# Optimization experiments

Measured on AMD Instinct MI355X. Metric: run time of the kernel, lower is better.

The kernel has to match this reference:

```python
import jax, jax.numpy as jnp
import numpy as np

B, S, D = 4, 2048, 2048
NH, NKV = 16, 4
HD = D // NH            # 128
DKV = NKV * HD          # 512
REP = NH // NKV         # 4
SCALE = HD ** -0.5
EPS = 1e-9


def setup_inputs() -> dict:
    key = jax.random.key(0)
    ks = jax.random.split(key, 9)
    s = 0.02
    return {
        "q": jax.random.normal(ks[0], (B, S, D), jnp.float32),
        "k": jax.random.normal(ks[1], (B, S, D), jnp.float32),
        "v": jax.random.normal(ks[2], (B, S, D), jnp.float32),
        "Wq": jax.random.normal(ks[3], (D, D), jnp.float32) * s,
        "bq": jnp.zeros((D,), jnp.float32),
        "Wk": jax.random.normal(ks[4], (D, DKV), jnp.float32) * s,
        "bk": jnp.zeros((DKV,), jnp.float32),
        "Wv": jax.random.normal(ks[5], (D, DKV), jnp.float32) * s,
        "bv": jnp.zeros((DKV,), jnp.float32),
    }


def reference(q, k, v, Wq, bq, Wk, bk, Wv, bv):
    # Dense projections (nn.Dense = x @ W + b)
    qh = q @ Wq + bq                      # (B, S, D)
    kh = k @ Wk + bk                      # (B, S, DKV)
    vh = v @ Wv + bv                      # (B, S, DKV)
    # Faithful to source: repeat along axis=-2 (the SEQUENCE axis)
    kh = jnp.repeat(kh, REP, axis=-2)     # (B, S*REP, DKV)
    vh = jnp.repeat(vh, REP, axis=-2)     # (B, S*REP, DKV)
    # flash_attention math: reshape to (B, S, NH, HD) -> (B, NH, S, HD)
    qh = qh.reshape(B, S, NH, HD).transpose(0, 2, 1, 3)
    kh = kh.reshape(B, S, NH, HD).transpose(0, 2, 1, 3)
    vh = vh.reshape(B, S, NH, HD).transpose(0, 2, 1, 3)
    attn = jnp.einsum("bhqd,bhkd->bhqk", qh, kh) * SCALE
    m = jnp.max(attn, axis=-1, keepdims=True)
    e = jnp.exp(attn - m)
    p = e / (jnp.sum(e, axis=-1, keepdims=True) + EPS)
    out = jnp.einsum("bhqk,bhkd->bhqd", p, vh)   # (B, NH, S, HD)
    return out.transpose(0, 2, 1, 3).reshape(B, S, D)
```

## Files before the change

kernel.cpp:

```cpp
#include <hip/hip_runtime.h>

#define B_    4
#define S_    2048
#define D_    2048
#define NH_   16
#define NKV_  4
#define HD_   128
#define DKV_  512
#define QSCALE_ ((float)(0.08838834764831845 * 1.4426950408889634))

typedef __attribute__((ext_vector_type(8))) short          bf16x8;
typedef __attribute__((ext_vector_type(8))) unsigned short us8;
typedef __attribute__((ext_vector_type(4))) unsigned short us4;
typedef __attribute__((ext_vector_type(4))) float          f32x4;

__device__ __forceinline__ unsigned short f2bf(float f) {
    union { float f; unsigned int u; } v; v.f = f;
    unsigned int u = v.u;
    u += 0x7fffu + ((u >> 16) & 1u);
    return (unsigned short)(u >> 16);
}

__device__ __forceinline__ unsigned int cvt_pk_bf16(float lo, float hi) {
    unsigned int r;
    asm volatile("v_cvt_pk_bf16_f32 %0, %1, %2" : "=v"(r) : "v"(lo), "v"(hi));
    return r;
}

#define GLOAD16(gp, lp) __builtin_amdgcn_global_load_lds(                      \
    (const __attribute__((address_space(1))) unsigned int*)(gp),              \
    (__attribute__((address_space(3))) unsigned int*)(lp), 16, 0, 0)

__device__ __forceinline__ void tr_body(
    const float* __restrict__ W, unsigned short* __restrict__ WT,
    int K, int N, int kb, int nb, float (*tile)[33])
{
    const int k0 = kb * 32, n0 = nb * 32;
    const int tx = threadIdx.x & 31, ty = threadIdx.x >> 5;
#pragma unroll
    for (int i = 0; i < 32; i += 8)
        tile[ty + i][tx] = W[(size_t)(k0 + ty + i) * N + n0 + tx];
    __syncthreads();
#pragma unroll
    for (int i = 0; i < 32; i += 8)
        WT[(size_t)(n0 + ty + i) * K + k0 + tx] = f2bf(tile[tx][ty + i]);
}

__global__ __launch_bounds__(256) void transpose_all(
    const float* __restrict__ Wq, const float* __restrict__ Wk,
    const float* __restrict__ Wv, unsigned short* __restrict__ WqT,
    unsigned short* __restrict__ WkT, unsigned short* __restrict__ WvT)
{
    __shared__ float tile[32][33];
    const int y = blockIdx.y;
    if (y < 64)       tr_body(Wq, WqT, D_, D_,   blockIdx.x, y,      tile);
    else if (y < 80)  tr_body(Wk, WkT, D_, DKV_, blockIdx.x, y - 64, tile);
    else              tr_body(Wv, WvT, D_, DKV_, blockIdx.x, y - 80, tile);
}

__device__ __forceinline__ void cvt_body(
    const float* __restrict__ src, unsigned short* __restrict__ dst, int n8)
{
    int i = blockIdx.x * blockDim.x + threadIdx.x;
    const int stride = gridDim.x * blockDim.x;
    const float4* p = (const float4*)src;
    us8* o8 = (us8*)dst;
    for (; i < n8; i += stride) {
        float4 a = p[2 * i], b = p[2 * i + 1];
        us8 o;
        o[0] = f2bf(a.x); o[1] = f2bf(a.y); o[2] = f2bf(a.z); o[3] = f2bf(a.w);
        o[4] = f2bf(b.x); o[5] = f2bf(b.y); o[6] = f2bf(b.z); o[7] = f2bf(b.w);
        o8[i] = o;
    }
}

__global__ __launch_bounds__(256) void cvt_bf16(
    const float* __restrict__ in, unsigned short* __restrict__ out, int n8)
{
    cvt_body(in, out, n8);
}

__global__ __launch_bounds__(256) void cvt_all(
    const float* __restrict__ q, const float* __restrict__ k,
    const float* __restrict__ v, unsigned short* __restrict__ xq,
    unsigned short* __restrict__ xk, unsigned short* __restrict__ xv)
{
    const int which = blockIdx.y;
    const float* src = which == 0 ? q : which == 1 ? k : v;
    unsigned short* dst = which == 0 ? xq : which == 1 ? xk : xv;
    cvt_body(src, dst, B_ * S_ * D_ / 8);
}

__device__ __forceinline__ void gemm_body(
    const unsigned short* __restrict__ A, const unsigned short* __restrict__ BT,
    const float* __restrict__ bias, unsigned short* __restrict__ C,
    int N, int nb, float scale, int vmode,
    unsigned short* As, unsigned short* Bs)
{
    const int K = D_;
    const int m0 = blockIdx.x * 128, n0 = nb * 128;
    const int t = threadIdx.x;
    const int w = t >> 6, l = t & 63, lr = l & 15, lg = l >> 4;
    const int wr = (w >> 1) * 64, wc = (w & 1) * 64;
    const int sr = t >> 2, sc = (t & 3) * 8;

    const unsigned short* aS = A + (size_t)(m0 + sr) * K + sc;
    const unsigned short* bS = BT + (size_t)(n0 + sr) * K + sc;

    f32x4 acc[4][4] = {};
    const int nk = K / 32;
    for (int kt = 0; kt < nk; ++kt) {
        __syncthreads();
        GLOAD16(aS + kt * 32,                    &As[t * 8]);
        GLOAD16(aS + (size_t)64 * K + kt * 32,   &As[2048 + t * 8]);
        GLOAD16(bS + kt * 32,                    &Bs[t * 8]);
        GLOAD16(bS + (size_t)64 * K + kt * 32,   &Bs[2048 + t * 8]);
        __syncthreads();

        bf16x8 af[4], bfv[4];
#pragma unroll
        for (int i = 0; i < 4; ++i)
            af[i] = *(const bf16x8*)&As[(wr + i * 16 + lr) * 32 + lg * 8];
#pragma unroll
        for (int i = 0; i < 4; ++i)
            bfv[i] = *(const bf16x8*)&Bs[(wc + i * 16 + lr) * 32 + lg * 8];
#pragma unroll
        for (int i = 0; i < 4; ++i)
#pragma unroll
            for (int j = 0; j < 4; ++j)
                acc[i][j] = __builtin_amdgcn_mfma_f32_16x16x32_bf16(
                    af[i], bfv[j], acc[i][j], 0, 0, 0);
    }

#pragma unroll
    for (int j = 0; j < 4; ++j) {
        const int col = n0 + wc + j * 16 + lr;
        const float bv = bias[col];
#pragma unroll
        for (int i = 0; i < 4; ++i) {
            const int row0 = m0 + wr + i * 16 + lg * 4;
            if (vmode == 0) {
#pragma unroll
                for (int r = 0; r < 4; ++r)
                    C[(size_t)(row0 + r) * N + col] = f2bf((acc[i][j][r] + bv) * scale);
            } else {
                const int bb = row0 >> 11, s0 = row0 & (S_ - 1);
                us4 hv;
#pragma unroll
                for (int r = 0; r < 4; ++r) hv[r] = f2bf((acc[i][j][r] + bv) * scale);
                *(us4*)&C[((size_t)bb * N + col) * S_ + s0] = hv;
            }
        }
    }
}

__global__ __launch_bounds__(256) void gemm_all(
    const unsigned short* __restrict__ xq, const unsigned short* __restrict__ xk,
    const unsigned short* __restrict__ xv,
    const unsigned short* __restrict__ WqT, const unsigned short* __restrict__ WkT,
    const unsigned short* __restrict__ WvT,
    const float* __restrict__ bq, const float* __restrict__ bk,
    const float* __restrict__ bv,
    unsigned short* __restrict__ qh, unsigned short* __restrict__ kh,
    unsigned short* __restrict__ vhT)
{
    __shared__ __align__(16) unsigned short As[128 * 32];
    __shared__ __align__(16) unsigned short Bs[128 * 32];
    const int y = blockIdx.y;
    if (y < 16)      gemm_body(xq, WqT, bq, qh,  D_,   y,      QSCALE_, 0, As, Bs);
    else if (y < 20) gemm_body(xk, WkT, bk, kh,  DKV_, y - 16, 1.0f,    0, As, Bs);
    else             gemm_body(xv, WvT, bv, vhT, DKV_, y - 20, 1.0f,    1, As, Bs);
}

__global__ __launch_bounds__(256) void gemm_lds(
    const unsigned short* __restrict__ A, const unsigned short* __restrict__ BT,
    const float* __restrict__ bias, unsigned short* __restrict__ C,
    int N, float scale, int vmode)
{
    __shared__ __align__(16) unsigned short As[128 * 32];
    __shared__ __align__(16) unsigned short Bs[128 * 32];
    gemm_body(A, BT, bias, C, N, blockIdx.y, scale, vmode, As, Bs);
}

template <int VMODE>
__global__ __launch_bounds__(256) void gemm_rs(
    const float* __restrict__ A, const unsigned short* __restrict__ BT,
    const float* __restrict__ bias, unsigned short* __restrict__ C,
    int M, int N, int K, float scale)
{
    __shared__ unsigned short As[128][40];
    __shared__ unsigned short Bs[128][40];

    const int m0 = blockIdx.x * 128, n0 = blockIdx.y * 128;
    const int t = threadIdx.x;
    const int sr = t >> 1, sc = (t & 1) * 16;
    const int w = t >> 6, l = t & 63, lr = l & 15, lg = l >> 4;
    const int wr = (w >> 1) * 64, wc = (w & 1) * 64;

    const float* aptr = A + (size_t)(m0 + sr) * K + sc;
    const unsigned short* bptr = BT + (size_t)(n0 + sr) * K + sc;

    float4 pa0, pa1, pa2, pa3;
    us8 pb0, pb1;
    auto prefetch = [&](int k0) {
        const float4* ap = (const float4*)(aptr + k0);
        pa0 = ap[0]; pa1 = ap[1]; pa2 = ap[2]; pa3 = ap[3];
        const us8* bp = (const us8*)(bptr + k0);
        pb0 = bp[0]; pb1 = bp[1];
    };

    f32x4 acc[4][4] = {};
    prefetch(0);
    const int nk = K / 32;
    for (int kt = 0; kt < nk; ++kt) {
        __syncthreads();
        us8 c0, c1;
        c0[0] = f2bf(pa0.x); c0[1] = f2bf(pa0.y); c0[2] = f2bf(pa0.z); c0[3] = f2bf(pa0.w);
        c0[4] = f2bf(pa1.x); c0[5] = f2bf(pa1.y); c0[6] = f2bf(pa1.z); c0[7] = f2bf(pa1.w);
        c1[0] = f2bf(pa2.x); c1[1] = f2bf(pa2.y); c1[2] = f2bf(pa2.z); c1[3] = f2bf(pa2.w);
        c1[4] = f2bf(pa3.x); c1[5] = f2bf(pa3.y); c1[6] = f2bf(pa3.z); c1[7] = f2bf(pa3.w);
        *(us8*)&As[sr][sc]     = c0;
        *(us8*)&As[sr][sc + 8] = c1;
        *(us8*)&Bs[sr][sc]     = pb0;
        *(us8*)&Bs[sr][sc + 8] = pb1;
        __syncthreads();
        if (kt + 1 < nk) prefetch((kt + 1) * 32);

        bf16x8 af[4], bfv[4];
#pragma unroll
        for (int i = 0; i < 4; ++i)
            af[i] = *(const bf16x8*)&As[wr + i * 16 + lr][lg * 8];
#pragma unroll
        for (int i = 0; i < 4; ++i)
            bfv[i] = *(const bf16x8*)&Bs[wc + i * 16 + lr][lg * 8];
#pragma unroll
        for (int i = 0; i < 4; ++i)
#pragma unroll
            for (int j = 0; j < 4; ++j)
                acc[i][j] = __builtin_amdgcn_mfma_f32_16x16x32_bf16(
                    af[i], bfv[j], acc[i][j], 0, 0, 0);
    }

#pragma unroll
    for (int j = 0; j < 4; ++j) {
        const int col = n0 + wc + j * 16 + lr;
        const float bv = bias[col];
#pragma unroll
        for (int i = 0; i < 4; ++i) {
            const int row0 = m0 + wr + i * 16 + lg * 4;
            if (VMODE == 0) {
#pragma unroll
                for (int r = 0; r < 4; ++r)
                    C[(size_t)(row0 + r) * N + col] = f2bf((acc[i][j][r] + bv) * scale);
            } else {
                const int bb = row0 >> 11, s0 = row0 & (S_ - 1);
                us4 hv;
#pragma unroll
                for (int r = 0; r < 4; ++r) hv[r] = f2bf((acc[i][j][r] + bv) * scale);
                *(us4*)&C[((size_t)bb * N + col) * S_ + s0] = hv;
            }
        }
    }
}

__global__ __launch_bounds__(256, 2) void attn_kernel(
    const unsigned short* __restrict__ qh, const unsigned short* __restrict__ kh,
    const unsigned short* __restrict__ vhT, float* __restrict__ out)
{
    __shared__ __align__(16) unsigned short Kd[2][64 * 128];
    __shared__ __align__(16) unsigned short Vd[2][128 * 64];
    __shared__ __align__(16) unsigned int   P2T[4][16 * 44];

    const int qb = blockIdx.x, h = blockIdx.y, b = blockIdx.z;
    const int g = h & (NKV_ - 1);
    const int t = threadIdx.x, w = t >> 6, l = t & 63, lr = l & 15, lg = l >> 4;
    const int q0 = qb * 128 + w * 32;

    bf16x8 qf[2][4];
#pragma unroll
    for (int rf = 0; rf < 2; ++rf) {
        const unsigned short* qrow =
            qh + ((size_t)(b * S_) + q0 + rf * 16 + lr) * D_ + h * HD_;
#pragma unroll
        for (int ko = 0; ko < 4; ++ko)
            qf[rf][ko] = *(const bf16x8*)(qrow + ko * 32 + lg * 8);
    }

    f32x4 o[2][8] = {};
    float mrow[2] = {-1e30f, -1e30f};
    float ls[2]   = {0.f, 0.f};

    const unsigned short* kb_ = kh + (size_t)b * S_ * DKV_ + g * HD_;
    const unsigned short* vb_ = vhT + ((size_t)b * DKV_ + g * HD_) * S_;

    const int kc = ((t & 15) * 8) ^ (((t >> 4) & 7) << 3);
    const int vc = ((t & 7) * 8) ^ (((t >> 3) & 7) << 3);

    auto stage = [&](int buf, int kt) {
        const unsigned short* ks = kb_ + (size_t)(kt * 64) * DKV_ + kc;
        const unsigned short* vs = vb_ + kt * 64 + vc;
#pragma unroll
        for (int i = 0; i < 4; ++i)
            GLOAD16(ks + (size_t)(i * 16 + (t >> 4)) * DKV_, &Kd[buf][i * 2048 + t * 8]);
#pragma unroll
        for (int i = 0; i < 4; ++i)
            GLOAD16(vs + (size_t)(i * 32 + (t >> 3)) * S_,   &Vd[buf][i * 2048 + t * 8]);
    };

    stage(0, 0);
    stage(1, 1);

    const int swz = (lr & 7) << 3;
    unsigned int* pw = &P2T[w][lr * 44];
    int cur = 0;
    const int NT = S_ / 64;
    for (int kt = 0; kt < NT; ++kt) {
        if (kt + 1 < NT) { asm volatile("s_waitcnt vmcnt(8)" ::: "memory"); }
        else             { asm volatile("s_waitcnt vmcnt(0)" ::: "memory"); }
        __builtin_amdgcn_s_barrier();
        __builtin_amdgcn_sched_barrier(0);

        f32x4 sa[2][4] = {};
        __builtin_amdgcn_s_setprio(1);
#pragma unroll
        for (int cf = 0; cf < 4; ++cf)
#pragma unroll
            for (int ko = 0; ko < 4; ++ko) {
                bf16x8 kf = *(const bf16x8*)
                    &Kd[cur][(cf * 16 + lr) * 128 + ((ko * 32 + lg * 8) ^ swz)];
                sa[0][cf] = __builtin_amdgcn_mfma_f32_16x16x32_bf16(kf, qf[0][ko], sa[0][cf], 0, 0, 0);
                sa[1][cf] = __builtin_amdgcn_mfma_f32_16x16x32_bf16(kf, qf[1][ko], sa[1][cf], 0, 0, 0);
            }
        __builtin_amdgcn_s_setprio(0);

        bf16x8 pa[2][2];
#pragma unroll
        for (int rf = 0; rf < 2; ++rf) {
            float mxl = fmaxf(fmaxf(fmaxf(sa[rf][0][0], sa[rf][0][1]),
                                    fmaxf(sa[rf][0][2], sa[rf][0][3])),
                              fmaxf(fmaxf(sa[rf][1][0], sa[rf][1][1]),
                                    fmaxf(sa[rf][1][2], sa[rf][1][3])));
            mxl = fmaxf(mxl, fmaxf(fmaxf(fmaxf(sa[rf][2][0], sa[rf][2][1]),
                                         fmaxf(sa[rf][2][2], sa[rf][2][3])),
                                   fmaxf(fmaxf(sa[rf][3][0], sa[rf][3][1]),
                                         fmaxf(sa[rf][3][2], sa[rf][3][3]))));
            float m = mrow[rf];
            if (!__all(mxl <= m + 8.f)) {
                float mx = fmaxf(mxl, m);
                mx = fmaxf(mx, __shfl_xor(mx, 16));
                mx = fmaxf(mx, __shfl_xor(mx, 32));
                const float al = exp2f(m - mx);
                mrow[rf] = m = mx;
                ls[rf] *= al;
#pragma unroll
                for (int r = 0; r < 4; ++r) {
                    const float a = __shfl(al, lg * 4 + r);
#pragma unroll
                    for (int df = 0; df < 8; ++df) o[rf][df][r] *= a;
                }
            }
            float p[4][4];
#pragma unroll
            for (int cf = 0; cf < 4; ++cf)
#pragma unroll
                for (int r = 0; r < 4; ++r)
                    p[cf][r] = exp2f(sa[rf][cf][r] - m);
            ls[rf] += ((p[0][0] + p[0][1]) + (p[0][2] + p[0][3]))
                    + ((p[1][0] + p[1][1]) + (p[1][2] + p[1][3]))
                    + ((p[2][0] + p[2][1]) + (p[2][2] + p[2][3]))
                    + ((p[3][0] + p[3][1]) + (p[3][2] + p[3][3]));
#pragma unroll
            for (int cf = 0; cf < 4; ++cf) {
                uint2 pk;
                pk.x = cvt_pk_bf16(p[cf][0], p[cf][1]);
                pk.y = cvt_pk_bf16(p[cf][2], p[cf][3]);
                *(uint2*)&pw[cf * 8 + lg * 2] = pk;
            }
            pa[rf][0] = *(const bf16x8*)&pw[lg * 4];
            pa[rf][1] = *(const bf16x8*)&pw[16 + lg * 4];
        }

        __builtin_amdgcn_s_setprio(1);
#pragma unroll
        for (int ks = 0; ks < 2; ++ks)
#pragma unroll
            for (int df = 0; df < 8; ++df) {
                bf16x8 vf = *(const bf16x8*)
                    &Vd[cur][(df * 16 + lr) * 64 + ((ks * 32 + lg * 8) ^ swz)];
                o[0][df] = __builtin_amdgcn_mfma_f32_16x16x32_bf16(pa[0][ks], vf, o[0][df], 0, 0, 0);
                o[1][df] = __builtin_amdgcn_mfma_f32_16x16x32_bf16(pa[1][ks], vf, o[1][df], 0, 0, 0);
            }
        __builtin_amdgcn_s_setprio(0);

        __builtin_amdgcn_sched_barrier(0);
        __builtin_amdgcn_s_barrier();
        __builtin_amdgcn_sched_barrier(0);
        if (kt + 2 < NT) stage(cur, kt + 2);
        cur ^= 1;
    }

#pragma unroll
    for (int rf = 0; rf < 2; ++rf) {
        float lst = ls[rf];
        lst += __shfl_xor(lst, 16);
        lst += __shfl_xor(lst, 32);
        const float inv = 1.f / (lst + 1e-9f);
        float* ob = out + ((size_t)(b * S_) + q0 + rf * 16 + lg * 4) * D_ + h * HD_;
#pragma unroll
        for (int r = 0; r < 4; ++r) {
            const float ivr = __shfl(inv, lg * 4 + r);
#pragma unroll
            for (int df = 0; df < 8; ++df)
                ob[(size_t)r * D_ + df * 16 + lr] = o[rf][df][r] * ivr;
        }
    }
}

extern "C" void kernel_launch(void* const* d_in, const int* in_sizes, int n_in,
                              void* d_out, int out_size, void* d_ws, size_t ws_size,
                              hipStream_t stream)
{
    const float* q  = (const float*)d_in[0];
    const float* k  = (const float*)d_in[1];
    const float* v  = (const float*)d_in[2];
    const float* Wq = (const float*)d_in[3];
    const float* bq = (const float*)d_in[4];
    const float* Wk = (const float*)d_in[5];
    const float* bk = (const float*)d_in[6];
    const float* Wv = (const float*)d_in[7];
    const float* bv = (const float*)d_in[8];
    float* out = (float*)d_out;

    char* ws = (char*)d_ws;
    unsigned short* qh  = (unsigned short*)ws; ws += (size_t)B_ * S_ * D_ * 2;
    unsigned short* kh  = (unsigned short*)ws; ws += (size_t)B_ * S_ * DKV_ * 2;
    unsigned short* vhT = (unsigned short*)ws; ws += (size_t)B_ * DKV_ * S_ * 2;
    unsigned short* WqT = (unsigned short*)ws; ws += (size_t)D_ * D_ * 2;
    unsigned short* WkT = (unsigned short*)ws; ws += (size_t)DKV_ * D_ * 2;
    unsigned short* WvT = (unsigned short*)ws; ws += (size_t)DKV_ * D_ * 2;
    unsigned short* xq  = (unsigned short*)ws; ws += (size_t)B_ * S_ * D_ * 2;
    unsigned short* xk  = (unsigned short*)ws; ws += (size_t)B_ * S_ * D_ * 2;
    unsigned short* xv  = (unsigned short*)ws; ws += (size_t)B_ * S_ * D_ * 2;

    const size_t need3 = (size_t)163577856;
    const size_t need1 = (size_t)96468992;

    transpose_all<<<dim3(64, 96), 256, 0, stream>>>(Wq, Wk, Wv, WqT, WkT, WvT);

    const int M = B_ * S_;
    const int n8 = M * D_ / 8;

    if (ws_size >= need3) {
        cvt_all<<<dim3(1024, 3), 256, 0, stream>>>(q, k, v, xq, xk, xv);
        gemm_all<<<dim3(M / 128, 24), 256, 0, stream>>>(
            xq, xk, xv, WqT, WkT, WvT, bq, bk, bv, qh, kh, vhT);
    } else if (ws_size >= need1) {
        cvt_bf16<<<2048, 256, 0, stream>>>(q, xq, n8);
        gemm_lds<<<dim3(M / 128, D_ / 128), 256, 0, stream>>>(xq, WqT, bq, qh, D_, QSCALE_, 0);
        cvt_bf16<<<2048, 256, 0, stream>>>(k, xq, n8);
        gemm_lds<<<dim3(M / 128, DKV_ / 128), 256, 0, stream>>>(xq, WkT, bk, kh, DKV_, 1.0f, 0);
        cvt_bf16<<<2048, 256, 0, stream>>>(v, xq, n8);
        gemm_lds<<<dim3(M / 128, DKV_ / 128), 256, 0, stream>>>(xq, WvT, bv, vhT, DKV_, 1.0f, 1);
    } else {
        gemm_rs<0><<<dim3(M / 128, D_ / 128), 256, 0, stream>>>(q, WqT, bq, qh, M, D_, D_, QSCALE_);
        gemm_rs<0><<<dim3(M / 128, DKV_ / 128), 256, 0, stream>>>(k, WkT, bk, kh, M, DKV_, D_, 1.0f);
        gemm_rs<1><<<dim3(M / 128, DKV_ / 128), 256, 0, stream>>>(v, WvT, bv, vhT, M, DKV_, D_, 1.0f);
    }

    attn_kernel<<<dim3(S_ / 128, NH_, B_), 256, 0, stream>>>(qh, kh, vhT, out);
}
```

Measured before the change: 414.5 us.

## Double-buffer projection GEMM LDS and compute softmax row sums via MFMA

The projection GEMM now double-buffers its LDS tiles, so the global-to-LDS copy for the next k-tile is issued before the current tile's MFMAs. This removes one barrier per iteration and doubles LDS use per block. In the attention kernel, the per-row softmax denominator is now accumulated by extra MFMAs against a vector of ones instead of VALU adds and cross-lane shuffles, which moves work onto the matrix units and sums the bf16-rounded probabilities. The row-max reduction also switches to v_max3 instructions to cut VALU op count.

```diff
diff --git a/kernel.cpp b/kernel.cpp
--- a/kernel.cpp
+++ b/kernel.cpp
@@ -24,6 +24,12 @@
 __device__ __forceinline__ unsigned int cvt_pk_bf16(float lo, float hi) {
     unsigned int r;
     asm volatile("v_cvt_pk_bf16_f32 %0, %1, %2" : "=v"(r) : "v"(lo), "v"(hi));
+    return r;
+}
+
+__device__ __forceinline__ float vmax3(float a, float b, float c) {
+    float r;
+    asm("v_max3_f32 %0, %1, %2, %3" : "=v"(r) : "v"(a), "v"(b), "v"(c));
     return r;
 }
 
@@ -95,7 +101,7 @@
     const unsigned short* __restrict__ A, const unsigned short* __restrict__ BT,
     const float* __restrict__ bias, unsigned short* __restrict__ C,
     int N, int nb, float scale, int vmode,
-    unsigned short* As, unsigned short* Bs)
+    unsigned short* As , unsigned short* Bs )
 {
     const int K = D_;
     const int m0 = blockIdx.x * 128, n0 = nb * 128;
@@ -107,29 +113,38 @@
     const unsigned short* aS = A + (size_t)(m0 + sr) * K + sc;
     const unsigned short* bS = BT + (size_t)(n0 + sr) * K + sc;
 
+    auto stage = [&](int buf, int kt) {
+        GLOAD16(aS + kt * 32,                    &As[buf * 4096 + t * 8]);
+        GLOAD16(aS + (size_t)64 * K + kt * 32,   &As[buf * 4096 + 2048 + t * 8]);
+        GLOAD16(bS + kt * 32,                    &Bs[buf * 4096 + t * 8]);
+        GLOAD16(bS + (size_t)64 * K + kt * 32,   &Bs[buf * 4096 + 2048 + t * 8]);
+    };
+
     f32x4 acc[4][4] = {};
+    stage(0, 0);
+    __syncthreads();
+
     const int nk = K / 32;
+    int cur = 0;
     for (int kt = 0; kt < nk; ++kt) {
-        __syncthreads();
-        GLOAD16(aS + kt * 32,                    &As[t * 8]);
-        GLOAD16(aS + (size_t)64 * K + kt * 32,   &As[2048 + t * 8]);
-        GLOAD16(bS + kt * 32,                    &Bs[t * 8]);
-        GLOAD16(bS + (size_t)64 * K + kt * 32,   &Bs[2048 + t * 8]);
-        __syncthreads();
+        if (kt + 1 < nk) stage(cur ^ 1, kt + 1);
 
         bf16x8 af[4], bfv[4];
 #pragma unroll
         for (int i = 0; i < 4; ++i)
-            af[i] = *(const bf16x8*)&As[(wr + i * 16 + lr) * 32 + lg * 8];
-#pragma unroll
-        for (int i = 0; i < 4; ++i)
-            bfv[i] = *(const bf16x8*)&Bs[(wc + i * 16 + lr) * 32 + lg * 8];
+            af[i] = *(const bf16x8*)&As[cur * 4096 + (wr + i * 16 + lr) * 32 + lg * 8];
+#pragma unroll
+        for (int i = 0; i < 4; ++i)
+            bfv[i] = *(const bf16x8*)&Bs[cur * 4096 + (wc + i * 16 + lr) * 32 + lg * 8];
 #pragma unroll
         for (int i = 0; i < 4; ++i)
 #pragma unroll
             for (int j = 0; j < 4; ++j)
                 acc[i][j] = __builtin_amdgcn_mfma_f32_16x16x32_bf16(
                     af[i], bfv[j], acc[i][j], 0, 0, 0);
+
+        __syncthreads();
+        cur ^= 1;
     }
 
 #pragma unroll
@@ -164,8 +179,8 @@
     unsigned short* __restrict__ qh, unsigned short* __restrict__ kh,
     unsigned short* __restrict__ vhT)
 {
-    __shared__ __align__(16) unsigned short As[128 * 32];
-    __shared__ __align__(16) unsigned short Bs[128 * 32];
+    __shared__ __align__(16) unsigned short As[2 * 128 * 32];
+    __shared__ __align__(16) unsigned short Bs[2 * 128 * 32];
     const int y = blockIdx.y;
     if (y < 16)      gemm_body(xq, WqT, bq, qh,  D_,   y,      QSCALE_, 0, As, Bs);
     else if (y < 20) gemm_body(xk, WkT, bk, kh,  DKV_, y - 16, 1.0f,    0, As, Bs);
@@ -177,8 +192,8 @@
     const float* __restrict__ bias, unsigned short* __restrict__ C,
     int N, float scale, int vmode)
 {
-    __shared__ __align__(16) unsigned short As[128 * 32];
-    __shared__ __align__(16) unsigned short Bs[128 * 32];
+    __shared__ __align__(16) unsigned short As[2 * 128 * 32];
+    __shared__ __align__(16) unsigned short Bs[2 * 128 * 32];
     gemm_body(A, BT, bias, C, N, blockIdx.y, scale, vmode, As, Bs);
 }
 
@@ -286,9 +301,13 @@
             qf[rf][ko] = *(const bf16x8*)(qrow + ko * 32 + lg * 8);
     }
 
+    bf16x8 onesf;
+#pragma unroll
+    for (int j = 0; j < 8; ++j) onesf[j] = (short)0x3F80;
+
     f32x4 o[2][8] = {};
+    f32x4 oe[2] = {};
     float mrow[2] = {-1e30f, -1e30f};
-    float ls[2]   = {0.f, 0.f};
 
     const unsigned short* kb_ = kh + (size_t)b * S_ * DKV_ + g * HD_;
     const unsigned short* vb_ = vhT + ((size_t)b * DKV_ + g * HD_) * S_;
@@ -336,14 +355,13 @@
         bf16x8 pa[2][2];
 #pragma unroll
         for (int rf = 0; rf < 2; ++rf) {
-            float mxl = fmaxf(fmaxf(fmaxf(sa[rf][0][0], sa[rf][0][1]),
-                                    fmaxf(sa[rf][0][2], sa[rf][0][3])),
-                              fmaxf(fmaxf(sa[rf][1][0], sa[rf][1][1]),
-                                    fmaxf(sa[rf][1][2], sa[rf][1][3])));
-            mxl = fmaxf(mxl, fmaxf(fmaxf(fmaxf(sa[rf][2][0], sa[rf][2][1]),
-                                         fmaxf(sa[rf][2][2], sa[rf][2][3])),
-                                   fmaxf(fmaxf(sa[rf][3][0], sa[rf][3][1]),
-                                         fmaxf(sa[rf][3][2], sa[rf][3][3]))));
+            const float m0v = vmax3(sa[rf][0][0], sa[rf][0][1], sa[rf][0][2]);
+            const float m1v = vmax3(sa[rf][0][3], sa[rf][1][0], sa[rf][1][1]);
+            const float m2v = vmax3(sa[rf][1][2], sa[rf][1][3], sa[rf][2][0]);
+            const float m3v = vmax3(sa[rf][2][1], sa[rf][2][2], sa[rf][2][3]);
+            const float m4v = vmax3(sa[rf][3][0], sa[rf][3][1], sa[rf][3][2]);
+            const float mxl = fmaxf(vmax3(m0v, m1v, m2v),
+                                    vmax3(m3v, m4v, sa[rf][3][3]));
             float m = mrow[rf];
             if (!__all(mxl <= m + 8.f)) {
                 float mx = fmaxf(mxl, m);
@@ -351,10 +369,10 @@
                 mx = fmaxf(mx, __shfl_xor(mx, 32));
                 const float al = exp2f(m - mx);
                 mrow[rf] = m = mx;
-                ls[rf] *= al;
 #pragma unroll
                 for (int r = 0; r < 4; ++r) {
                     const float a = __shfl(al, lg * 4 + r);
+                    oe[rf][r] *= a;
 #pragma unroll
                     for (int df = 0; df < 8; ++df) o[rf][df][r] *= a;
                 }
@@ -365,10 +383,6 @@
 #pragma unroll
                 for (int r = 0; r < 4; ++r)
                     p[cf][r] = exp2f(sa[rf][cf][r] - m);
-            ls[rf] += ((p[0][0] + p[0][1]) + (p[0][2] + p[0][3]))
-                    + ((p[1][0] + p[1][1]) + (p[1][2] + p[1][3]))
-                    + ((p[2][0] + p[2][1]) + (p[2][2] + p[2][3]))
-                    + ((p[3][0] + p[3][1]) + (p[3][2] + p[3][3]));
 #pragma unroll
             for (int cf = 0; cf < 4; ++cf) {
                 uint2 pk;
@@ -390,6 +404,10 @@
                 o[0][df] = __builtin_amdgcn_mfma_f32_16x16x32_bf16(pa[0][ks], vf, o[0][df], 0, 0, 0);
                 o[1][df] = __builtin_amdgcn_mfma_f32_16x16x32_bf16(pa[1][ks], vf, o[1][df], 0, 0, 0);
             }
+        oe[0] = __builtin_amdgcn_mfma_f32_16x16x32_bf16(pa[0][0], onesf, oe[0], 0, 0, 0);
+        oe[0] = __builtin_amdgcn_mfma_f32_16x16x32_bf16(pa[0][1], onesf, oe[0], 0, 0, 0);
+        oe[1] = __builtin_amdgcn_mfma_f32_16x16x32_bf16(pa[1][0], onesf, oe[1], 0, 0, 0);
+        oe[1] = __builtin_amdgcn_mfma_f32_16x16x32_bf16(pa[1][1], onesf, oe[1], 0, 0, 0);
         __builtin_amdgcn_s_setprio(0);
 
         __builtin_amdgcn_sched_barrier(0);
@@ -401,17 +419,13 @@
 
 #pragma unroll
     for (int rf = 0; rf < 2; ++rf) {
-        float lst = ls[rf];
-        lst += __shfl_xor(lst, 16);
-        lst += __shfl_xor(lst, 32);
-        const float inv = 1.f / (lst + 1e-9f);
         float* ob = out + ((size_t)(b * S_) + q0 + rf * 16 + lg * 4) * D_ + h * HD_;
 #pragma unroll
         for (int r = 0; r < 4; ++r) {
-            const float ivr = __shfl(inv, lg * 4 + r);
+            const float inv = 1.f / (oe[rf][r] + 1e-9f);
 #pragma unroll
             for (int df = 0; df < 8; ++df)
-                ob[(size_t)r * D_ + df * 16 + lr] = o[rf][df][r] * ivr;
+                ob[(size_t)r * D_ + df * 16 + lr] = o[rf][df][r] * inv;
         }
     }
 }
```

After: 395.6 us. 4.6% less time.
